# Optimization experiments

Measured on AMD Instinct MI355X. Metric: run time of the kernel, lower is better.

The kernel has to match this reference:

```python
import jax, jax.numpy as jnp
import numpy as np

ROPE_BASE = 10000.0

def _rope_cos_sin(T, dh, dtype):
    inv_freq = 1.0 / (ROPE_BASE ** (jnp.arange(0, dh, 2, dtype=jnp.float32) / dh))
    t = jnp.arange(T, dtype=jnp.float32)
    freqs = jnp.outer(t, inv_freq)                      # [T, dh/2]
    emb = jnp.concatenate([freqs, freqs], axis=-1)      # [T, dh]
    return jnp.cos(emb).astype(dtype), jnp.sin(emb).astype(dtype)

def _rotate_half(x):
    x1, x2 = jnp.split(x, 2, axis=-1)
    return jnp.concatenate([-x2, x1], axis=-1)

def setup_inputs() -> dict:
    key = jax.random.key(0)
    k1, k2, k3 = jax.random.split(key, 3)
    B, T, D = 2, 2048, 2048
    x = jax.random.normal(k1, (B, T, D), dtype=jnp.float32)
    w_qkv = jax.random.normal(k2, (3 * D, D), dtype=jnp.float32) * (D ** -0.5)
    w_proj = jax.random.normal(k3, (D, D), dtype=jnp.float32) * (D ** -0.5)
    return {"x": x, "w_qkv": w_qkv, "w_proj": w_proj}

def reference(x, w_qkv, w_proj):
    B, T, D = x.shape
    H = 16
    Dh = D // H
    scale = Dh ** -0.5
    qkv = x @ w_qkv.T                                   # [B,T,3D]
    qkv = qkv.reshape(B, T, 3, H, Dh).transpose(2, 0, 3, 1, 4)  # [3,B,H,T,Dh]
    q, k, v = qkv[0], qkv[1], qkv[2]
    cos, sin = _rope_cos_sin(T, Dh, x.dtype)            # [T,Dh] each, offset=0
    q = q * cos + _rotate_half(q) * sin
    k = k * cos + _rotate_half(k) * sin
    attn = jnp.einsum('bhqd,bhkd->bhqk', q, k) * scale  # [B,H,T,T]
    causal = jnp.triu(jnp.full((T, T), -jnp.inf, dtype=attn.dtype), k=1)
    attn = jax.nn.softmax(attn + causal, axis=-1)
    out = jnp.einsum('bhqk,bhkd->bhqd', attn, v)        # [B,H,T,Dh]
    out = out.transpose(0, 2, 1, 3).reshape(B, T, D)
    return out @ w_proj.T
```

## Files before the change

### kernel.cpp

```cpp
#include <hip/hip_runtime.h>
#include <stdint.h>

typedef unsigned short u16;
typedef unsigned int   u32;
typedef __attribute__((ext_vector_type(8))) __bf16 bf16x8;
typedef __attribute__((ext_vector_type(4))) float  f32x4;

#define MFMA_16x16x32_BF16(a, b, c) __builtin_amdgcn_mfma_f32_16x16x32_bf16((a), (b), (c), 0, 0, 0)

__device__ __forceinline__ u16 f2b(float f) {
    u32 u = __builtin_bit_cast(u32, f);
    u32 r = (u + 0x7FFFu + ((u >> 16) & 1u)) >> 16;
    return (u16)r;
}
__device__ __forceinline__ float b2f(u16 h) {
    u32 u = ((u32)h) << 16;
    return __builtin_bit_cast(float, u);
}

__device__ __forceinline__ void gload_lds16(const void* g, void* l) {
    __builtin_amdgcn_global_load_lds(
        (const __attribute__((address_space(1))) u32*)g,
        (__attribute__((address_space(3))) u32*)l,
        16, 0, 0);
}

__global__ __launch_bounds__(256) void cast3(const float* __restrict__ x,
                                             const float* __restrict__ wq,
                                             const float* __restrict__ wp,
                                             u16* __restrict__ xb,
                                             u16* __restrict__ wqb,
                                             u16* __restrict__ wpb) {
    const int n1 = 8388608, n2 = 12582912, n3 = 4194304;
    const int total4 = (n1 + n2 + n3) / 4;
    for (int i = blockIdx.x * blockDim.x + threadIdx.x; i < total4;
         i += gridDim.x * blockDim.x) {
        int e = i * 4;
        const float* src; u16* dst; int off;
        if (e < n1)            { src = x;  dst = xb;  off = e; }
        else if (e < n1 + n2)  { src = wq; dst = wqb; off = e - n1; }
        else                   { src = wp; dst = wpb; off = e - n1 - n2; }
        float4 v = *(const float4*)(src + off);
        ushort4 o;
        o.x = f2b(v.x); o.y = f2b(v.y); o.z = f2b(v.z); o.w = f2b(v.w);
        *(ushort4*)(dst + off) = o;
    }
}

template <int OUT_BF16>
__global__ __launch_bounds__(256) void gemm_bt(const u16* __restrict__ A,
                                               const u16* __restrict__ Bt,
                                               void* __restrict__ Cout,
                                               int M, int N, int K) {
    __shared__ u16 Al[128 * 64];
    __shared__ u16 Bl[128 * 64];
    const int tid  = threadIdx.x;
    const int w    = tid >> 6;
    const int lane = tid & 63;
    const int quad = lane >> 4;
    const int l16  = lane & 15;
    const int m0 = blockIdx.y * 128;
    const int n0 = blockIdx.x * 128;
    const int wm = (w >> 1) * 64;
    const int wn = (w & 1) * 64;

    f32x4 acc[4][4];
#pragma unroll
    for (int i = 0; i < 4; i++) {
#pragma unroll
        for (int j = 0; j < 4; j++) acc[i][j] = (f32x4){0.f, 0.f, 0.f, 0.f};
    }

    const int srow = tid >> 3;
    const int scol = ((tid & 7) ^ (srow & 7)) * 8;
    const u16* Abase = A + (size_t)(m0 + srow) * K + scol;
    const u16* Bbase = Bt + (size_t)(n0 + srow) * K + scol;
    char* AlB = (char*)Al + w * 1024;
    char* BlB = (char*)Bl + w * 1024;
    const int fx = (l16 & 7);

    for (int k0 = 0; k0 < K; k0 += 64) {
        __syncthreads();
#pragma unroll
        for (int i = 0; i < 4; i++) {
            gload_lds16(Abase + (size_t)i * 32 * K + k0, AlB + i * 4096);
            gload_lds16(Bbase + (size_t)i * 32 * K + k0, BlB + i * 4096);
        }
        __syncthreads();
#pragma unroll
        for (int ks = 0; ks < 2; ks++) {
            const int cb = ((ks * 4 + quad) ^ fx) * 8;
            bf16x8 Af[4];
#pragma unroll
            for (int mi = 0; mi < 4; mi++)
                Af[mi] = *(const bf16x8*)&Al[(wm + mi * 16 + l16) * 64 + cb];
#pragma unroll
            for (int ni = 0; ni < 4; ni++) {
                bf16x8 Bf = *(const bf16x8*)&Bl[(wn + ni * 16 + l16) * 64 + cb];
#pragma unroll
                for (int mi = 0; mi < 4; mi++)
                    acc[mi][ni] = MFMA_16x16x32_BF16(Af[mi], Bf, acc[mi][ni]);
            }
        }
    }

    const int row0 = m0 + wm + quad * 4;
    const int col0 = n0 + wn + l16;
#pragma unroll
    for (int mi = 0; mi < 4; mi++) {
#pragma unroll
        for (int r = 0; r < 4; r++) {
            size_t rowb = (size_t)(row0 + mi * 16 + r) * N;
#pragma unroll
            for (int ni = 0; ni < 4; ni++) {
                float v = acc[mi][ni][r];
                if (OUT_BF16) ((u16*)Cout)[rowb + col0 + ni * 16] = f2b(v);
                else          ((float*)Cout)[rowb + col0 + ni * 16] = v;
            }
        }
    }
}

__global__ __launch_bounds__(256) void rope_qk(const u16* __restrict__ qkv,
                                               u16* __restrict__ Q,
                                               u16* __restrict__ K) {
    const int bt = blockIdx.x;
    const int b = bt >> 11, t = bt & 2047;
    const u16* row = qkv + (size_t)bt * 6144;
    const int tid = threadIdx.x;

#pragma unroll
    for (int it = 0; it < 8; it++) {
        int p   = it * 256 + tid;
        int qk  = p >> 10;
        int rem = p & 1023;
        int h   = rem >> 6;
        int i   = rem & 63;
        float x1 = b2f(row[qk * 2048 + h * 128 + i]);
        float x2 = b2f(row[qk * 2048 + h * 128 + i + 64]);
        float inv = __expf(-0.14391156f * (float)i);
        float th  = (float)t * inv;
        float s, c;
        sincosf(th, &s, &c);
        float o1 = x1 * c - x2 * s;
        float o2 = x2 * c + x1 * s;
        u16* dst = (qk ? K : Q) + ((size_t)((b * 16 + h) * 2048 + t)) * 128;
        dst[i]      = f2b(o1);
        dst[i + 64] = f2b(o2);
    }
}

__global__ __launch_bounds__(256) void vtrans(const u16* __restrict__ qkv,
                                              u16* __restrict__ VT) {
    __shared__ u16 S[64 * 136];
    const int tc = blockIdx.x;
    const int bh = blockIdx.y;
    const int b = bh >> 4, h = bh & 15;
    const int tid = threadIdx.x;

#pragma unroll
    for (int i = 0; i < 4; i++) {
        int idx = i * 256 + tid;
        int t  = idx >> 4;
        int d8 = (idx & 15) * 8;
        uint4 v = *(const uint4*)(qkv + ((size_t)(b * 2048 + tc * 64 + t)) * 6144
                                      + 4096 + h * 128 + d8);
        *(uint4*)&S[t * 136 + d8] = v;
    }
    __syncthreads();
#pragma unroll
    for (int i = 0; i < 4; i++) {
        int idx = i * 256 + tid;
        int d  = idx >> 3;
        int t8 = (idx & 7) * 8;
        u16 tmp[8];
#pragma unroll
        for (int j = 0; j < 8; j++) tmp[j] = S[(t8 + j) * 136 + d];
        *(uint4*)(VT + ((size_t)(bh * 128 + d)) * 2048 + tc * 64 + t8) = *(uint4*)tmp;
    }
}

__global__ __launch_bounds__(256) void attn(const u16* __restrict__ Q,
                                            const u16* __restrict__ Kg,
                                            const u16* __restrict__ VTg,
                                            u16* __restrict__ O) {
    __shared__ u16 Kl[2][64 * 128];
    __shared__ u16 Vt[2][128 * 64];
    __shared__ u16 Pl[4 * 16 * 76];

    const int tid  = threadIdx.x;
    const int w    = tid >> 6;
    const int lane = tid & 63;
    const int quad = lane >> 4;
    const int l16  = lane & 15;
    const int pair = blockIdx.x;
    const int bh   = blockIdx.y;
    const int b = bh >> 4, h = bh & 15;
    const size_t base = (size_t)bh * 2048 * 128;
    const u16* Qb  = Q + base;
    const u16* Kb  = Kg + base;
    const u16* VTb = VTg + base;
    u16* Plw = Pl + w * 16 * 76;
    const float scale = 0.08838834764831845f;

    const int krow = tid >> 4;
    const int kcol = (((tid & 15) ^ (krow & 7)) * 8);
    const int vrow = w * 8 + (lane >> 3);
    const int vcol = (((lane & 7) ^ (vrow & 7)) * 8);
    const int fx   = (l16 & 7);

    for (int s = 0; s < 2; s++) {
        const int qt   = s ? (31 - pair) : pair;
        const int q0   = qt * 64;
        const int row0 = q0 + w * 16;

        bf16x8 Qf[4];
#pragma unroll
        for (int kk = 0; kk < 4; kk++)
            Qf[kk] = *(const bf16x8*)&Qb[(size_t)(row0 + l16) * 128 + kk * 32 + quad * 8];

        f32x4 Oacc[8];
#pragma unroll
        for (int ni = 0; ni < 8; ni++) Oacc[ni] = (f32x4){0.f, 0.f, 0.f, 0.f};
        float mrow = -1e30f, lrow = 0.f;

        const int nkt = qt + 1;

        __syncthreads();
        {
            const u16* ksrc = Kb + (size_t)krow * 128 + kcol;
            char* kdst = (char*)Kl[0] + w * 1024;
            const u16* vsrc = VTb + (size_t)vrow * 2048 + vcol;
            char* vdst = (char*)Vt[0] + w * 1024;
#pragma unroll
            for (int i = 0; i < 4; i++) {
                gload_lds16(ksrc + (size_t)i * 16 * 128, kdst + i * 4096);
                gload_lds16(vsrc + (size_t)i * 32 * 2048, vdst + i * 4096);
            }
        }

        for (int kt = 0; kt < nkt; kt++) {
            const int kt0 = kt * 64;
            const int cur = kt & 1;
            __syncthreads();

            if (kt + 1 < nkt) {
                const int kt1 = kt0 + 64;
                const u16* ksrc = Kb + (size_t)(kt1 + krow) * 128 + kcol;
                char* kdst = (char*)Kl[cur ^ 1] + w * 1024;
                const u16* vsrc = VTb + (size_t)vrow * 2048 + kt1 + vcol;
                char* vdst = (char*)Vt[cur ^ 1] + w * 1024;
#pragma unroll
                for (int i = 0; i < 4; i++) {
                    gload_lds16(ksrc + (size_t)i * 16 * 128, kdst + i * 4096);
                    gload_lds16(vsrc + (size_t)i * 32 * 2048, vdst + i * 4096);
                }
            }

            const u16* Klc = Kl[cur];
            const u16* Vtc = Vt[cur];

            f32x4 ST[4];
#pragma unroll
            for (int mi = 0; mi < 4; mi++) ST[mi] = (f32x4){0.f, 0.f, 0.f, 0.f};
#pragma unroll
            for (int kk = 0; kk < 4; kk++) {
                const int cb = ((kk * 4 + quad) ^ fx) * 8;
#pragma unroll
                for (int mi = 0; mi < 4; mi++) {
                    bf16x8 Kf = *(const bf16x8*)&Klc[(mi * 16 + l16) * 128 + cb];
                    ST[mi] = MFMA_16x16x32_BF16(Kf, Qf[kk], ST[mi]);
                }
            }

            const bool needs_mask = (kt0 + 63) > row0;
            const int qg = row0 + l16;
            float tmax = -1e30f;
#pragma unroll
            for (int mi = 0; mi < 4; mi++) {
#pragma unroll
                for (int r = 0; r < 4; r++) {
                    float sv = ST[mi][r] * scale;
                    if (needs_mask) {
                        int kg = kt0 + mi * 16 + quad * 4 + r;
                        sv = (kg > qg) ? -1e30f : sv;
                    }
                    ST[mi][r] = sv;
                    tmax = fmaxf(tmax, sv);
                }
            }
            tmax = fmaxf(tmax, __shfl_xor(tmax, 16));
            tmax = fmaxf(tmax, __shfl_xor(tmax, 32));

            if (__any(tmax > mrow + 8.0f)) {
                float mnew  = fmaxf(mrow, tmax);
                float alpha = __expf(mrow - mnew);
                mrow = mnew;
                lrow *= alpha;
                float aRow[4];
#pragma unroll
                for (int r = 0; r < 4; r++) aRow[r] = __shfl(alpha, quad * 4 + r);
#pragma unroll
                for (int ni = 0; ni < 8; ni++) {
#pragma unroll
                    for (int r = 0; r < 4; r++) Oacc[ni][r] *= aRow[r];
                }
            }

            float tsum = 0.f;
#pragma unroll
            for (int mi = 0; mi < 4; mi++) {
#pragma unroll
                for (int r = 0; r < 4; r++) {
                    float p = __expf(ST[mi][r] - mrow);
                    ST[mi][r] = p;
                    tsum += p;
                }
            }
            lrow += tsum;

#pragma unroll
            for (int mi = 0; mi < 4; mi++) {
                ushort4 pk;
                pk.x = f2b(ST[mi][0]); pk.y = f2b(ST[mi][1]);
                pk.z = f2b(ST[mi][2]); pk.w = f2b(ST[mi][3]);
                *(ushort4*)&Plw[l16 * 76 + mi * 16 + quad * 4] = pk;
            }

            bf16x8 Pf[2];
#pragma unroll
            for (int kk = 0; kk < 2; kk++)
                Pf[kk] = *(const bf16x8*)&Plw[l16 * 76 + kk * 32 + quad * 8];
#pragma unroll
            for (int kk = 0; kk < 2; kk++) {
                const int cb = ((kk * 4 + quad) ^ fx) * 8;
#pragma unroll
                for (int ni = 0; ni < 8; ni++) {
                    bf16x8 Vf = *(const bf16x8*)&Vtc[(ni * 16 + l16) * 64 + cb];
                    Oacc[ni] = MFMA_16x16x32_BF16(Pf[kk], Vf, Oacc[ni]);
                }
            }
        }

        lrow += __shfl_xor(lrow, 16);
        lrow += __shfl_xor(lrow, 32);
        float inv = 1.0f / lrow;
        float iRow[4];
#pragma unroll
        for (int r = 0; r < 4; r++) iRow[r] = __shfl(inv, quad * 4 + r);

#pragma unroll
        for (int r = 0; r < 4; r++) {
            int t = row0 + quad * 4 + r;
            size_t rowb = ((size_t)(b * 2048 + t)) * 2048 + (size_t)(h * 128);
#pragma unroll
            for (int ni = 0; ni < 8; ni++)
                O[rowb + ni * 16 + l16] = f2b(Oacc[ni][r] * iRow[r]);
        }
    }
}

extern "C" void kernel_launch(void* const* d_in, const int* in_sizes, int n_in,
                              void* d_out, int out_size, void* d_ws, size_t ws_size,
                              hipStream_t stream) {
    const float* x  = (const float*)d_in[0];
    const float* wq = (const float*)d_in[1];
    const float* wp = (const float*)d_in[2];

    char* ws = (char*)d_ws;
    u16* xb   = (u16*)(ws + 0);
    u16* wqb  = (u16*)(ws + 16777216);
    u16* wpb  = (u16*)(ws + 41943040);
    u16* qkvb = (u16*)(ws + 50331648);
    u16* Qr   = (u16*)(ws + 100663296);
    u16* Kr   = (u16*)(ws + 117440512);
    u16* VTt  = (u16*)(ws + 134217728);
    u16* Ob   = (u16*)(ws + 50331648);
    if (ws_size < 150994944) return;

    cast3<<<2048, 256, 0, stream>>>(x, wq, wp, xb, wqb, wpb);
    gemm_bt<1><<<dim3(48, 32), 256, 0, stream>>>(xb, wqb, qkvb, 4096, 6144, 2048);
    rope_qk<<<4096, 256, 0, stream>>>(qkvb, Qr, Kr);
    vtrans<<<dim3(32, 32), 256, 0, stream>>>(qkvb, VTt);
    attn<<<dim3(16, 32), 256, 0, stream>>>(Qr, Kr, VTt, Ob);
    gemm_bt<0><<<dim3(16, 32), 256, 0, stream>>>(Ob, wpb, (float*)d_out, 4096, 2048, 2048);
}
```

Measured before the change: 407.2 us.

## Read V fragments directly from global memory and vectorize RoPE with shared sin/cos table

The attention kernel no longer stages the transposed V tile in LDS. Each PV MFMA now loads its V fragment directly from global memory, which removes the LDS traffic and halves the shared-memory footprint, possibly raising occupancy. The cost is uncoalesced, unprefetched global loads inside the inner loop, which are exposed to global latency. Separately, the RoPE kernel computes sin/cos once per position into shared memory and uses 16-byte vector loads and stores in place of scalar ones.

```diff
diff --git a/kernel.cpp b/kernel.cpp
--- a/kernel.cpp
+++ b/kernel.cpp
@@ -124,30 +124,40 @@
 __global__ __launch_bounds__(256) void rope_qk(const u16* __restrict__ qkv,
                                                u16* __restrict__ Q,
                                                u16* __restrict__ K) {
+    __shared__ float cs[64], sn[64];
     const int bt = blockIdx.x;
     const int b = bt >> 11, t = bt & 2047;
     const u16* row = qkv + (size_t)bt * 6144;
     const int tid = threadIdx.x;
 
-#pragma unroll
-    for (int it = 0; it < 8; it++) {
-        int p   = it * 256 + tid;
-        int qk  = p >> 10;
-        int rem = p & 1023;
-        int h   = rem >> 6;
-        int i   = rem & 63;
-        float x1 = b2f(row[qk * 2048 + h * 128 + i]);
-        float x2 = b2f(row[qk * 2048 + h * 128 + i + 64]);
-        float inv = __expf(-0.14391156f * (float)i);
-        float th  = (float)t * inv;
+    if (tid < 64) {
+        float inv = __expf(-0.14391156f * (float)tid);
         float s, c;
-        sincosf(th, &s, &c);
-        float o1 = x1 * c - x2 * s;
-        float o2 = x2 * c + x1 * s;
-        u16* dst = (qk ? K : Q) + ((size_t)((b * 16 + h) * 2048 + t)) * 128;
-        dst[i]      = f2b(o1);
-        dst[i + 64] = f2b(o2);
-    }
+        sincosf((float)t * inv, &s, &c);
+        sn[tid] = s; cs[tid] = c;
+    }
+    __syncthreads();
+
+    const int qk = tid >> 7;
+    const int h  = (tid >> 3) & 15;
+    const int i0 = (tid & 7) * 8;
+    const u16* src = row + qk * 2048 + h * 128;
+    uint4 a  = *(const uint4*)(src + i0);
+    uint4 b4 = *(const uint4*)(src + i0 + 64);
+    const u16* pa = (const u16*)&a;
+    const u16* pb = (const u16*)&b4;
+    u16 o1[8], o2[8];
+#pragma unroll
+    for (int j = 0; j < 8; j++) {
+        int i = i0 + j;
+        float x1 = b2f(pa[j]), x2 = b2f(pb[j]);
+        float s = sn[i], c = cs[i];
+        o1[j] = f2b(x1 * c - x2 * s);
+        o2[j] = f2b(x2 * c + x1 * s);
+    }
+    u16* dst = (qk ? K : Q) + ((size_t)((b * 16 + h) * 2048 + t)) * 128;
+    *(uint4*)(dst + i0)      = *(uint4*)o1;
+    *(uint4*)(dst + i0 + 64) = *(uint4*)o2;
 }
 
 __global__ __launch_bounds__(256) void vtrans(const u16* __restrict__ qkv,
@@ -185,7 +195,6 @@
                                             const u16* __restrict__ VTg,
                                             u16* __restrict__ O) {
     __shared__ u16 Kl[2][64 * 128];
-    __shared__ u16 Vt[2][128 * 64];
     __shared__ u16 Pl[4 * 16 * 76];
 
     const int tid  = threadIdx.x;
@@ -205,8 +214,6 @@
 
     const int krow = tid >> 4;
     const int kcol = (((tid & 15) ^ (krow & 7)) * 8);
-    const int vrow = w * 8 + (lane >> 3);
-    const int vcol = (((lane & 7) ^ (vrow & 7)) * 8);
     const int fx   = (l16 & 7);
 
     for (int s = 0; s < 2; s++) {
@@ -230,13 +237,9 @@
         {
             const u16* ksrc = Kb + (size_t)krow * 128 + kcol;
             char* kdst = (char*)Kl[0] + w * 1024;
-            const u16* vsrc = VTb + (size_t)vrow * 2048 + vcol;
-            char* vdst = (char*)Vt[0] + w * 1024;
-#pragma unroll
-            for (int i = 0; i < 4; i++) {
+#pragma unroll
+            for (int i = 0; i < 4; i++)
                 gload_lds16(ksrc + (size_t)i * 16 * 128, kdst + i * 4096);
-                gload_lds16(vsrc + (size_t)i * 32 * 2048, vdst + i * 4096);
-            }
         }
 
         for (int kt = 0; kt < nkt; kt++) {
@@ -248,17 +251,12 @@
                 const int kt1 = kt0 + 64;
                 const u16* ksrc = Kb + (size_t)(kt1 + krow) * 128 + kcol;
                 char* kdst = (char*)Kl[cur ^ 1] + w * 1024;
-                const u16* vsrc = VTb + (size_t)vrow * 2048 + kt1 + vcol;
-                char* vdst = (char*)Vt[cur ^ 1] + w * 1024;
-#pragma unroll
-                for (int i = 0; i < 4; i++) {
+#pragma unroll
+                for (int i = 0; i < 4; i++)
                     gload_lds16(ksrc + (size_t)i * 16 * 128, kdst + i * 4096);
-                    gload_lds16(vsrc + (size_t)i * 32 * 2048, vdst + i * 4096);
-                }
             }
 
             const u16* Klc = Kl[cur];
-            const u16* Vtc = Vt[cur];
 
             f32x4 ST[4];
 #pragma unroll
@@ -333,10 +331,11 @@
                 Pf[kk] = *(const bf16x8*)&Plw[l16 * 76 + kk * 32 + quad * 8];
 #pragma unroll
             for (int kk = 0; kk < 2; kk++) {
-                const int cb = ((kk * 4 + quad) ^ fx) * 8;
+                const int cbg = (kk * 4 + quad) * 8;
 #pragma unroll
                 for (int ni = 0; ni < 8; ni++) {
-                    bf16x8 Vf = *(const bf16x8*)&Vtc[(ni * 16 + l16) * 64 + cb];
+                    bf16x8 Vf = *(const bf16x8*)
+                        &VTb[(size_t)(ni * 16 + l16) * 2048 + kt0 + cbg];
                     Oacc[ni] = MFMA_16x16x32_BF16(Pf[kk], Vf, Oacc[ni]);
                 }
             }
```

Measured after the change: 472.3 us. +16.0%, slower.
